# Kernel tuning notes

Measured on AMD Instinct MI355X. Metric: run time of the kernel, lower is better.

Reference implementation:

```python
import jax, jax.numpy as jnp
import numpy as np

N_SOTU, N_TAXON, N_EDGES, H = 100000, 50000, 1000000, 128

def setup_inputs() -> dict:
    key = jax.random.key(0)
    ks = jax.random.split(key, 8)
    return {
        "z_sotu": jax.random.normal(ks[0], (N_SOTU, H), dtype=jnp.float32),
        "z_taxon": jax.random.normal(ks[1], (N_TAXON, H), dtype=jnp.float32),
        "row": jax.random.randint(ks[2], (N_EDGES,), 0, N_SOTU, dtype=jnp.int64),
        "col": jax.random.randint(ks[3], (N_EDGES,), 0, N_TAXON, dtype=jnp.int64),
        "w1": jax.random.normal(ks[4], (H, 2 * H), dtype=jnp.float32) * 0.05,
        "b1": jax.random.normal(ks[5], (H,), dtype=jnp.float32) * 0.05,
        "w2": jax.random.normal(ks[6], (1, H), dtype=jnp.float32) * 0.05,
        "b2": jax.random.normal(ks[7], (1,), dtype=jnp.float32) * 0.05,
    }

def reference(z_sotu, z_taxon, row, col, w1, b1, w2, b2):
    # Gather edge endpoints and concat: [E, 2H]
    z = jnp.concatenate([z_sotu[row], z_taxon[col]], axis=-1)
    # 2-layer MLP (torch Linear: y = x @ W.T + b)
    h = jax.nn.relu(jnp.einsum('eh,oh->eo', z, w1) + b1)
    out = jnp.einsum('eh,oh->eo', h, w2) + b2
    return out.reshape(-1)
```

## Files before the change

kernel.cpp:

```cpp
#include <hip/hip_runtime.h>
#include <hip/hip_bf16.h>


#define HID  128
#define FTE  128
#define PST  136
#define PTR  32
#define GU   1024
#define GT   512

typedef __attribute__((ext_vector_type(8)))  short    bf16x8;
typedef __attribute__((ext_vector_type(16))) float    f32x16;
typedef __attribute__((ext_vector_type(4)))  unsigned uint4v;

__device__ __forceinline__ float bf2f(unsigned short u) {
    return __uint_as_float(((unsigned)u) << 16);
}
__device__ __forceinline__ unsigned pk2(float x, float y) {
    __hip_bfloat162 t = __float22bfloat162_rn(make_float2(x, y));
    return *reinterpret_cast<unsigned*>(&t);
}
__device__ __forceinline__ bf16x8 pack8(float4 a, float4 b) {
    uint4v r;
    r.x = pk2(a.x, a.y); r.y = pk2(a.z, a.w);
    r.z = pk2(b.x, b.y); r.w = pk2(b.z, b.w);
    return *reinterpret_cast<bf16x8*>(&r);
}

__global__ __launch_bounds__(256)
void prep_kernel(const float* __restrict__ zs, const float* __restrict__ zt,
                 const float* __restrict__ w1, const float* __restrict__ b1,
                 unsigned short* __restrict__ U, unsigned short* __restrict__ V,
                 int NS, int NT)
{
    __shared__ __align__(16) unsigned short zl[2][PTR * PST];

    const bool isU = (int)blockIdx.x < GU;
    const float* z      = isU ? zs : zt;
    unsigned short* O   = isU ? U  : V;
    const int N    = isU ? NS : NT;
    const int nT   = (N + PTR - 1) / PTR;
    const int t0   = isU ? blockIdx.x : blockIdx.x - GU;
    const int step = isU ? GU : GT;
    const int koff = isU ? 0 : 128;

    const int tid  = threadIdx.x;
    const int wave = tid >> 6;
    const int lane = tid & 63;
    const int l31  = lane & 31;
    const int hlf  = lane >> 5;

    if (t0 >= nT) return;

    float4 ra[4];

    auto stage_load = [&](int t) {
        #pragma unroll
        for (int i = 0; i < 2; ++i) {
            const int f = i * 256 + tid;
            const int r = f >> 4;
            const int c = f & 15;
            int s = t * PTR + r;
            if (s >= N) s = N - 1;
            const float* src = z + (long long)s * HID + c * 8;
            ra[2*i]     = *(const float4*)(src);
            ra[2*i + 1] = *(const float4*)(src + 4);
        }
    };
    auto stage_write = [&](unsigned short* buf) {
        #pragma unroll
        for (int i = 0; i < 2; ++i) {
            const int f = i * 256 + tid;
            const int r = f >> 4;
            const int c = f & 15;
            *(bf16x8*)(buf + r * PST + c * 8) = pack8(ra[2*i], ra[2*i + 1]);
        }
    };

    stage_load(t0);

    bf16x8 afrag[8];
    {
        const float* wrow = w1 + (32 * wave + l31) * 256 + koff + hlf * 8;
        #pragma unroll
        for (int ks = 0; ks < 8; ++ks) {
            const float4 a = *(const float4*)(wrow + ks * 16);
            const float4 b = *(const float4*)(wrow + ks * 16 + 4);
            afrag[ks] = pack8(a, b);
        }
    }
    float b1v[16];
    #pragma unroll
    for (int g = 0; g < 4; ++g) {
        const int hb = 32 * wave + 8 * g + 4 * hlf;
        if (isU) {
            const float4 bb = *(const float4*)(b1 + hb);
            b1v[4*g+0] = bb.x; b1v[4*g+1] = bb.y; b1v[4*g+2] = bb.z; b1v[4*g+3] = bb.w;
        } else {
            b1v[4*g+0] = b1v[4*g+1] = b1v[4*g+2] = b1v[4*g+3] = 0.0f;
        }
    }
    stage_write(zl[0]);
    __syncthreads();

    int p = 0;
    for (int t = t0; t < nT; ) {
        const int tn = t + step;
        const bool pf = (tn < nT);

        if (pf) stage_load(tn);

        f32x16 acc = {};
        #pragma unroll
        for (int ks = 0; ks < 8; ++ks) {
            const bf16x8 bfrag = *(const bf16x8*)(zl[p] + l31 * PST + (2 * ks + hlf) * 8);
            acc = __builtin_amdgcn_mfma_f32_32x32x16_bf16(afrag[ks], bfrag, acc, 0, 0, 0);
        }
        const int s = t * PTR + l31;
        if (s < N) {
            #pragma unroll
            for (int g = 0; g < 4; ++g) {
                const int cb = 32 * wave + 8 * g + 4 * hlf;
                uint2 o;
                o.x = pk2(acc[4*g+0] + b1v[4*g+0], acc[4*g+1] + b1v[4*g+1]);
                o.y = pk2(acc[4*g+2] + b1v[4*g+2], acc[4*g+3] + b1v[4*g+3]);
                *(uint2*)(O + (long long)s * HID + cb) = o;
            }
        }

        if (pf) stage_write(zl[p ^ 1]);

        __syncthreads();
        p ^= 1;
        t = tn;
    }
}

__global__ __launch_bounds__(256)
void edge_kernel(const unsigned short* __restrict__ U,
                 const unsigned short* __restrict__ V,
                 const int*   __restrict__ row, const int* __restrict__ col,
                 const float* __restrict__ w2, const float* __restrict__ b2,
                 float* __restrict__ out, int E)
{
    const int tid = threadIdx.x;
    const int g   = tid >> 4;
    const int c16 = tid & 15;

    const long long eb = (long long)blockIdx.x * 64 + g * 4;

    int ri[4], ci[4];
    #pragma unroll
    for (int j = 0; j < 4; ++j) {
        long long e = eb + j;
        if (e >= E) e = E - 1;
        ri[j] = row[e]; ci[j] = col[e];
    }
    bf16x8 u[4], v[4];
    #pragma unroll
    for (int j = 0; j < 4; ++j) {
        u[j] = *(const bf16x8*)(U + (long long)ri[j] * HID + c16 * 8);
        v[j] = *(const bf16x8*)(V + (long long)ci[j] * HID + c16 * 8);
    }

    const float4 wa = *(const float4*)(w2 + c16 * 8);
    const float4 wb = *(const float4*)(w2 + c16 * 8 + 4);
    const float w2v[8] = {wa.x, wa.y, wa.z, wa.w, wb.x, wb.y, wb.z, wb.w};

    float p[4] = {0.0f, 0.0f, 0.0f, 0.0f};
    #pragma unroll
    for (int j = 0; j < 4; ++j) {
        #pragma unroll
        for (int k = 0; k < 8; ++k) {
            const float h = fmaxf(bf2f((unsigned short)u[j][k]) +
                                  bf2f((unsigned short)v[j][k]), 0.0f);
            p[j] = fmaf(h, w2v[k], p[j]);
        }
    }
    #pragma unroll
    for (int d = 1; d < 16; d <<= 1) {
        #pragma unroll
        for (int j = 0; j < 4; ++j) p[j] += __shfl_xor(p[j], d, 64);
    }
    if (c16 == 0) {
        const float bb = b2[0];
        if (eb + 3 < E) {
            *(float4*)(out + eb) = make_float4(p[0] + bb, p[1] + bb, p[2] + bb, p[3] + bb);
        } else {
            #pragma unroll
            for (int j = 0; j < 4; ++j)
                if (eb + j < E) out[eb + j] = p[j] + bb;
        }
    }
}

__global__ __launch_bounds__(256, 2)
void edge_mlp_fused(const float* __restrict__ z_sotu, const float* __restrict__ z_taxon,
                    const int* __restrict__ row, const int* __restrict__ col,
                    const float* __restrict__ w1, const float* __restrict__ b1,
                    const float* __restrict__ w2, const float* __restrict__ b2,
                    float* __restrict__ out, int E)
{
    __shared__ __align__(16) unsigned short zsh[FTE * 256];
    const int tid  = threadIdx.x;
    const int wave = tid >> 6;
    const int lane = tid & 63;
    const int l31  = lane & 31;
    const int hlf  = lane >> 5;
    const long long e0 = (long long)blockIdx.x * FTE;
    {
        const int ch  = lane & 15;
        const int rhl = lane >> 4;
        #pragma unroll
        for (int pass = 0; pass < 16; ++pass) {
            const int rh = pass * 4 + rhl;
            const int r  = 32 * wave + (rh >> 1);
            const int hh = rh & 1;
            long long e = e0 + r;
            if (e >= E) e = E - 1;
            const int idx = hh ? col[e] : row[e];
            const float* src = (hh ? z_taxon : z_sotu) + (long long)idx * HID + ch * 8;
            const float4 a = *(const float4*)(src);
            const float4 b = *(const float4*)(src + 4);
            const int c = hh * 16 + ch;
            const int q = c ^ (r & 31);
            *(bf16x8*)(zsh + r * 256 + q * 8) = pack8(a, b);
        }
    }
    bf16x8 afrag[16];
    {
        const float* wrow = w1 + (32 * wave + l31) * 256 + hlf * 8;
        #pragma unroll
        for (int ks = 0; ks < 16; ++ks) {
            const float4 a = *(const float4*)(wrow + ks * 16);
            const float4 b = *(const float4*)(wrow + ks * 16 + 4);
            afrag[ks] = pack8(a, b);
        }
    }
    __syncthreads();
    f32x16 acc[4] = {};
    #pragma unroll
    for (int ks = 0; ks < 16; ++ks) {
        #pragma unroll
        for (int nt = 0; nt < 4; ++nt) {
            const int el = 32 * nt + l31;
            const int q  = (2 * ks + hlf) ^ l31;
            bf16x8 bfrag = *(const bf16x8*)(zsh + el * 256 + q * 8);
            acc[nt] = __builtin_amdgcn_mfma_f32_32x32x16_bf16(afrag[ks], bfrag, acc[nt], 0, 0, 0);
        }
    }
    __syncthreads();
    float* partial = (float*)zsh;
    float b1v[16], w2v[16];
    #pragma unroll
    for (int g = 0; g < 4; ++g) {
        const int hb = 32 * wave + 8 * g + 4 * hlf;
        const float4 bb = *(const float4*)(b1 + hb);
        const float4 ww = *(const float4*)(w2 + hb);
        b1v[4*g+0] = bb.x; b1v[4*g+1] = bb.y; b1v[4*g+2] = bb.z; b1v[4*g+3] = bb.w;
        w2v[4*g+0] = ww.x; w2v[4*g+1] = ww.y; w2v[4*g+2] = ww.z; w2v[4*g+3] = ww.w;
    }
    #pragma unroll
    for (int nt = 0; nt < 4; ++nt) {
        float p = 0.0f;
        #pragma unroll
        for (int r = 0; r < 16; ++r) {
            const float h = fmaxf(acc[nt][r] + b1v[r], 0.0f);
            p = fmaf(h, w2v[r], p);
        }
        p += __shfl_xor(p, 32, 64);
        if (hlf == 0)
            partial[wave * FTE + 32 * nt + l31] = p;
    }
    __syncthreads();
    if (tid < FTE) {
        const long long e = e0 + tid;
        if (e < E) {
            out[e] = partial[0 * FTE + tid] + partial[1 * FTE + tid]
                   + partial[2 * FTE + tid] + partial[3 * FTE + tid]
                   + b2[0];
        }
    }
}

extern "C" void kernel_launch(void* const* d_in, const int* in_sizes, int n_in,
                              void* d_out, int out_size, void* d_ws, size_t ws_size,
                              hipStream_t stream) {
    const float* z_sotu  = (const float*)d_in[0];
    const float* z_taxon = (const float*)d_in[1];
    const int*   row     = (const int*)d_in[2];
    const int*   col     = (const int*)d_in[3];
    const float* w1      = (const float*)d_in[4];
    const float* b1      = (const float*)d_in[5];
    const float* w2      = (const float*)d_in[6];
    const float* b2      = (const float*)d_in[7];
    float*       out     = (float*)d_out;

    const int NS = in_sizes[0] / HID;
    const int NT = in_sizes[1] / HID;
    const int E  = in_sizes[2];
    const size_t need = ((size_t)NS + NT) * HID * 2;

    if (ws_size >= need) {
        unsigned short* U  = (unsigned short*)d_ws;
        unsigned short* Vv = U + (size_t)NS * HID;
        hipLaunchKernelGGL(prep_kernel, dim3(GU + GT), dim3(256), 0, stream,
                           z_sotu, z_taxon, w1, b1, U, Vv, NS, NT);
        const int nblocks = (E + 63) / 64;
        hipLaunchKernelGGL(edge_kernel, dim3(nblocks), dim3(256), 0, stream,
                           U, Vv, row, col, w2, b2, out, E);
    } else {
        const int nblocks = (E + FTE - 1) / FTE;
        hipLaunchKernelGGL(edge_mlp_fused, dim3(nblocks), dim3(256), 0, stream,
                           z_sotu, z_taxon, row, col, w1, b1, w2, b2, out, E);
    }
}
```

Baseline: 198.3 us.

## Prepack W1 into bf16 MFMA fragments and coalesce U/V stores via LDS

```diff
diff --git a/kernel.cpp b/kernel.cpp
--- a/kernel.cpp
+++ b/kernel.cpp
@@ -28,8 +28,25 @@
 }
 
 __global__ __launch_bounds__(256)
+void w1prep_kernel(const float* __restrict__ w1, unsigned short* __restrict__ WF)
+{
+    const int tau = blockIdx.x * 256 + threadIdx.x;
+    const int ks  = tau & 7;
+    const int lc  = tau >> 3;
+    const int h   = lc >> 8;
+    const int w   = (lc >> 6) & 3;
+    const int ln  = lc & 63;
+    const int l31 = ln & 31;
+    const int hlf = ln >> 5;
+    const float* src = w1 + (32 * w + l31) * 256 + h * 128 + hlf * 8 + ks * 16;
+    const float4 a = *(const float4*)(src);
+    const float4 b = *(const float4*)(src + 4);
+    *(bf16x8*)(WF + lc * 64 + ks * 8) = pack8(a, b);
+}
+
+__global__ __launch_bounds__(256)
 void prep_kernel(const float* __restrict__ zs, const float* __restrict__ zt,
-                 const float* __restrict__ w1, const float* __restrict__ b1,
+                 const unsigned short* __restrict__ WF, const float* __restrict__ b1,
                  unsigned short* __restrict__ U, unsigned short* __restrict__ V,
                  int NS, int NT)
 {
@@ -42,7 +59,6 @@
     const int nT   = (N + PTR - 1) / PTR;
     const int t0   = isU ? blockIdx.x : blockIdx.x - GU;
     const int step = isU ? GU : GT;
-    const int koff = isU ? 0 : 128;
 
     const int tid  = threadIdx.x;
     const int wave = tid >> 6;
@@ -81,13 +97,10 @@
 
     bf16x8 afrag[8];
     {
-        const float* wrow = w1 + (32 * wave + l31) * 256 + koff + hlf * 8;
-        #pragma unroll
-        for (int ks = 0; ks < 8; ++ks) {
-            const float4 a = *(const float4*)(wrow + ks * 16);
-            const float4 b = *(const float4*)(wrow + ks * 16 + 4);
-            afrag[ks] = pack8(a, b);
-        }
+        const unsigned short* wfb = WF + ((((isU ? 0 : 4) + wave) * 64) + lane) * 64;
+        #pragma unroll
+        for (int ks = 0; ks < 8; ++ks)
+            afrag[ks] = *(const bf16x8*)(wfb + ks * 8);
     }
     float b1v[16];
     #pragma unroll
@@ -116,16 +129,28 @@
             const bf16x8 bfrag = *(const bf16x8*)(zl[p] + l31 * PST + (2 * ks + hlf) * 8);
             acc = __builtin_amdgcn_mfma_f32_32x32x16_bf16(afrag[ks], bfrag, acc, 0, 0, 0);
         }
-        const int s = t * PTR + l31;
-        if (s < N) {
-            #pragma unroll
-            for (int g = 0; g < 4; ++g) {
-                const int cb = 32 * wave + 8 * g + 4 * hlf;
-                uint2 o;
-                o.x = pk2(acc[4*g+0] + b1v[4*g+0], acc[4*g+1] + b1v[4*g+1]);
-                o.y = pk2(acc[4*g+2] + b1v[4*g+2], acc[4*g+3] + b1v[4*g+3]);
-                *(uint2*)(O + (long long)s * HID + cb) = o;
-            }
+        __syncthreads();
+
+        unsigned short* E = zl[p];
+        #pragma unroll
+        for (int g = 0; g < 4; ++g) {
+            const int cb = 32 * wave + 8 * g + 4 * hlf;
+            uint2 o;
+            o.x = pk2(acc[4*g+0] + b1v[4*g+0], acc[4*g+1] + b1v[4*g+1]);
+            o.y = pk2(acc[4*g+2] + b1v[4*g+2], acc[4*g+3] + b1v[4*g+3]);
+            *(uint2*)(E + l31 * PST + cb) = o;
+        }
+        __syncthreads();
+
+        #pragma unroll
+        for (int i = 0; i < 2; ++i) {
+            const int f = i * 256 + tid;
+            const int r = f >> 4;
+            const int c = f & 15;
+            const int s2 = t * PTR + r;
+            if (s2 < N)
+                *(uint4v*)(O + (long long)s2 * HID + c * 8) =
+                    *(const uint4v*)(E + r * PST + c * 8);
         }
 
         if (pf) stage_write(zl[p ^ 1]);
@@ -299,13 +324,15 @@
     const int NS = in_sizes[0] / HID;
     const int NT = in_sizes[1] / HID;
     const int E  = in_sizes[2];
-    const size_t need = ((size_t)NS + NT) * HID * 2;
+    const size_t need = ((size_t)NS + NT) * HID * 2 + 65536;
 
     if (ws_size >= need) {
         unsigned short* U  = (unsigned short*)d_ws;
         unsigned short* Vv = U + (size_t)NS * HID;
+        unsigned short* WF = Vv + (size_t)NT * HID;
+        hipLaunchKernelGGL(w1prep_kernel, dim3(16), dim3(256), 0, stream, w1, WF);
         hipLaunchKernelGGL(prep_kernel, dim3(GU + GT), dim3(256), 0, stream,
-                           z_sotu, z_taxon, w1, b1, U, Vv, NS, NT);
+                           z_sotu, z_taxon, WF, b1, U, Vv, NS, NT);
         const int nblocks = (E + 63) / 64;
         hipLaunchKernelGGL(edge_kernel, dim3(nblocks), dim3(256), 0, stream,
                            U, Vv, row, col, w2, b2, out, E);
```

New measurement: 190.6 us. 3.9% less time.
